# Optimization experiments

Measured on AMD Instinct MI355X. Metric: run time of the kernel, lower is better.

The kernel has to match this reference:

```python
import jax, jax.numpy as jnp
import numpy as np

NUM_CHANNELS = 512
B_DIM = 64
C_DIM = 16
N = 512
FEAT = NUM_CHANNELS * 4 * 4  # 8192


def setup_inputs() -> dict:
    key = jax.random.key(0)
    k1, k2 = jax.random.split(key)
    inp = jax.random.normal(k1, (N, NUM_CHANNELS, 4, 4), dtype=jnp.float32)
    T = jax.random.normal(k2, (FEAT, B_DIM * C_DIM), dtype=jnp.float32) * 0.1
    return {"inp": inp, "T": T}


def reference(inp, T):
    x = inp.reshape(-1, FEAT)                      # (N, 8192)
    M = (x @ T).reshape(-1, B_DIM, C_DIM)          # (N, B, C)
    # pairwise L1 distance over C: (N, N, B)
    dist = jnp.sum(jnp.abs(M[:, None, :, :] - M[None, :, :, :]), axis=-1)
    o = jnp.sum(jnp.exp(-dist), axis=1)            # (N, B)
    return jnp.concatenate((x, o), axis=1)         # (N, 8192 + B)
```

## Files before the change

kernel.cpp:

```cpp
#include <hip/hip_runtime.h>

#define NROWS 512
#define FEAT  8192
#define BDIM  64
#define CDIM  16
#define MCOLS 1024
#define OUTC  8256
#define KSPLIT 16
#define KCHUNK (FEAT / KSPLIT)
#define MSIZE  (NROWS * MCOLS)

typedef __bf16 bf16x8 __attribute__((ext_vector_type(8)));
typedef float  floatx4 __attribute__((ext_vector_type(4)));

#define AS1 __attribute__((address_space(1)))
#define AS3 __attribute__((address_space(3)))

static __device__ __forceinline__ void gload16(const void* g, void* l) {
    __builtin_amdgcn_global_load_lds((AS1 void*)(g), (AS3 void*)(l), 16, 0, 0);
}

static __device__ __forceinline__ unsigned short f2bf(float f) {
    unsigned int x = __builtin_bit_cast(unsigned int, f);
    unsigned int r = (x + 0x7FFFu + ((x >> 16) & 1u)) >> 16;
    return (unsigned short)r;
}

__global__ __launch_bounds__(256) void prep_kernel(const float* __restrict__ x,
                                                   const float* __restrict__ T,
                                                   unsigned short* __restrict__ xb,
                                                   unsigned short* __restrict__ Tt,
                                                   float* __restrict__ out) {
    __shared__ float lds[64][65];
    int bid = blockIdx.x, t = threadIdx.x;
    if (bid < 4096) {
        int gid = bid * 256 + t;
        float4 v = *(const float4*)(x + (size_t)gid * 4);
        ushort4 u;
        u.x = f2bf(v.x); u.y = f2bf(v.y); u.z = f2bf(v.z); u.w = f2bf(v.w);
        *(ushort4*)(xb + (size_t)gid * 4) = u;
        int row = gid >> 11, col4 = gid & 2047;
        *(float4*)(out + (size_t)row * OUTC + col4 * 4) = v;
    } else {
        int b2 = bid - 4096;
        int kt = b2 & 127, nt = b2 >> 7;
        int kk = t >> 2, q = t & 3;
#pragma unroll
        for (int p = 0; p < 4; ++p) {
            int c4 = q + p * 4;
            float4 v = *(const float4*)(T + (size_t)(kt * 64 + kk) * MCOLS + nt * 64 + c4 * 4);
            lds[kk][c4 * 4 + 0] = v.x; lds[kk][c4 * 4 + 1] = v.y;
            lds[kk][c4 * 4 + 2] = v.z; lds[kk][c4 * 4 + 3] = v.w;
        }
        __syncthreads();
        int nr = t >> 2, ck = t & 3;
        unsigned int w[8];
#pragma unroll
        for (int j = 0; j < 8; ++j) {
            unsigned int lo = f2bf(lds[ck * 16 + j * 2 + 0][nr]);
            unsigned int hi = f2bf(lds[ck * 16 + j * 2 + 1][nr]);
            w[j] = lo | (hi << 16);
        }
        uint4* dst = (uint4*)(Tt + (size_t)(nt * 64 + nr) * FEAT + kt * 64 + ck * 16);
        dst[0] = make_uint4(w[0], w[1], w[2], w[3]);
        dst[1] = make_uint4(w[4], w[5], w[6], w[7]);
    }
}

__global__ __launch_bounds__(256, 2) void gemm_kernel(const unsigned short* __restrict__ xb,
                                                      const unsigned short* __restrict__ Tt,
                                                      float* __restrict__ Mp) {
    __shared__ __align__(16) unsigned short ldsA[128 * 32];
    __shared__ __align__(16) unsigned short ldsB[128 * 32];

    int bid = blockIdx.x;
    int mt = bid & 3, nt = (bid >> 2) & 7, ks = bid >> 5;
    int m0 = mt * 128, n0 = nt * 128, kbase = ks * KCHUNK;
    int t = threadIdx.x, w = t >> 6, l = t & 63;

    int r0 = w * 32 + (l >> 2);
    int c  = (l & 3) ^ ((r0 >> 1) & 3);
    const unsigned short* gA0 = xb + (size_t)(m0 + r0) * FEAT + kbase + c * 8;
    const unsigned short* gB0 = Tt + (size_t)(n0 + r0) * FEAT + kbase + c * 8;
    unsigned short* lA0 = &ldsA[w * 1024];
    unsigned short* lA1 = &ldsA[w * 1024 + 512];
    unsigned short* lB0 = &ldsB[w * 1024];
    unsigned short* lB1 = &ldsB[w * 1024 + 512];

    int wr = w >> 1, wc = w & 1, fm = l & 15, fq = l >> 4;
    int swz = (fm >> 1) & 3;
    const unsigned short* pa[4];
    const unsigned short* pb[4];
#pragma unroll
    for (int a = 0; a < 4; ++a)
        pa[a] = &ldsA[(wr * 64 + a * 16 + fm) * 32 + ((fq ^ swz) * 8)];
#pragma unroll
    for (int b = 0; b < 4; ++b)
        pb[b] = &ldsB[(wc * 64 + b * 16 + fm) * 32 + ((fq ^ swz) * 8)];

    floatx4 acc[4][4] = {};

    for (int kk = 0; kk < KCHUNK; kk += 32) {
        if (kk) __syncthreads();
        gload16(gA0 + kk,             lA0);
        gload16(gA0 + 16 * FEAT + kk, lA1);
        gload16(gB0 + kk,             lB0);
        gload16(gB0 + 16 * FEAT + kk, lB1);
        __syncthreads();
        bf16x8 af[4], bfr[4];
#pragma unroll
        for (int a = 0; a < 4; ++a) af[a] = *(const bf16x8*)pa[a];
#pragma unroll
        for (int b = 0; b < 4; ++b) bfr[b] = *(const bf16x8*)pb[b];
#pragma unroll
        for (int a = 0; a < 4; ++a)
#pragma unroll
            for (int b = 0; b < 4; ++b)
                acc[a][b] = __builtin_amdgcn_mfma_f32_16x16x32_bf16(af[a], bfr[b], acc[a][b], 0, 0, 0);
    }

    float* outp = Mp + (size_t)ks * MSIZE;
    int gr0 = m0 + wr * 64, gc0 = n0 + wc * 64;
#pragma unroll
    for (int a = 0; a < 4; ++a)
#pragma unroll
        for (int r = 0; r < 4; ++r) {
            int row = gr0 + a * 16 + fq * 4 + r;
#pragma unroll
            for (int b = 0; b < 4; ++b)
                outp[(size_t)row * MCOLS + gc0 + b * 16 + fm] = acc[a][b][r];
        }
}

__global__ __launch_bounds__(256) void reduce_kernel(const float* __restrict__ Mp,
                                                     float* __restrict__ Ms) {
    int gid = blockIdx.x * 256 + threadIdx.x;
    const float4* p = (const float4*)Mp;
    float4 s = p[gid];
#pragma unroll
    for (int k = 1; k < KSPLIT; ++k) {
        float4 v = p[(size_t)k * (MSIZE / 4) + gid];
        s.x += v.x; s.y += v.y; s.z += v.z; s.w += v.w;
    }
    ((float4*)Ms)[gid] = s;
}

__global__ __launch_bounds__(256) void pairwise_kernel(const float* __restrict__ Ms,
                                                       float* __restrict__ out) {
    __shared__ float ldsM[NROWS * 20];
    __shared__ float partial[4][64];
    int b = blockIdx.x & 63, it = blockIdx.x >> 6;
    int t = threadIdx.x;
#pragma unroll
    for (int p = 0; p < 8; ++p) {
        int idx = t + p * 256;
        int j = idx >> 2, c4 = idx & 3;
        float4 v = *(const float4*)(Ms + (size_t)j * MCOLS + b * CDIM + c4 * 4);
        *(float4*)&ldsM[j * 20 + c4 * 4] = v;
    }
    __syncthreads();

    int lane = t & 63, w = t >> 6;
    int i = it * 64 + lane;
    float mi[CDIM];
#pragma unroll
    for (int cc = 0; cc < CDIM; ++cc) mi[cc] = ldsM[i * 20 + cc];

    float acc = 0.0f;
    for (int jj = w * 128; jj < w * 128 + 128; ++jj) {
        float d = 0.0f;
#pragma unroll
        for (int cc = 0; cc < CDIM; ++cc) d += fabsf(mi[cc] - ldsM[jj * 20 + cc]);
        acc += __expf(-d);
    }
    partial[w][lane] = acc;
    __syncthreads();
    if (w == 0) {
        float o = partial[0][lane] + partial[1][lane] + partial[2][lane] + partial[3][lane];
        out[(size_t)i * OUTC + FEAT + b] = o;
    }
}

extern "C" void kernel_launch(void* const* d_in, const int* in_sizes, int n_in,
                              void* d_out, int out_size, void* d_ws, size_t ws_size,
                              hipStream_t stream) {
    const float* x = (const float*)d_in[0];
    const float* T = (const float*)d_in[1];
    float* out = (float*)d_out;

    unsigned short* xb = (unsigned short*)d_ws;
    unsigned short* Tt = (unsigned short*)((char*)d_ws + (8u << 20));
    float*          Mp = (float*)((char*)d_ws + (24u << 20));
    float*          Ms = (float*)((char*)d_ws + (56u << 20));

    prep_kernel<<<6144, 256, 0, stream>>>(x, T, xb, Tt, out);
    gemm_kernel<<<512, 256, 0, stream>>>(xb, Tt, Mp);
    reduce_kernel<<<512, 256, 0, stream>>>(Mp, Ms);
    pairwise_kernel<<<512, 256, 0, stream>>>(Ms, out);
}
```

Baseline: 137.1 us.

## Fuse all stages into one cooperative kernel with grid syncs

Merges the prep, GEMM, split-K reduce and pairwise stages into a single persistent cooperative kernel of 256 blocks by 512 threads, separated by grid-wide barriers, to remove three kernel launch gaps. The GEMM split-K factor is halved to 8, which cuts partial-sum traffic and the reduce work but leaves each block a longer K loop. The fallback path keeps four separate launches. Grid.sync barriers add their own overhead, and using only 256 blocks may underfill the device during the prep and pairwise phases.

```diff
diff --git a/kernel.cpp b/kernel.cpp
--- a/kernel.cpp
+++ b/kernel.cpp
@@ -1,4 +1,7 @@
 #include <hip/hip_runtime.h>
+#include <hip/hip_cooperative_groups.h>
+
+namespace cg = cooperative_groups;
 
 #define NROWS 512
 #define FEAT  8192
@@ -6,9 +9,11 @@
 #define CDIM  16
 #define MCOLS 1024
 #define OUTC  8256
-#define KSPLIT 16
+#define KSPLIT 8
 #define KCHUNK (FEAT / KSPLIT)
 #define MSIZE  (NROWS * MCOLS)
+
+#define SMEM_BYTES 43008
 
 typedef __bf16 bf16x8 __attribute__((ext_vector_type(8)));
 typedef float  floatx4 __attribute__((ext_vector_type(4)));
@@ -26,115 +31,114 @@
     return (unsigned short)r;
 }
 
-__global__ __launch_bounds__(256) void prep_kernel(const float* __restrict__ x,
-                                                   const float* __restrict__ T,
-                                                   unsigned short* __restrict__ xb,
-                                                   unsigned short* __restrict__ Tt,
-                                                   float* __restrict__ out) {
-    __shared__ float lds[64][65];
-    int bid = blockIdx.x, t = threadIdx.x;
-    if (bid < 4096) {
-        int gid = bid * 256 + t;
+
+static __device__ __forceinline__ void prep_body(
+        int bid, int t, char* smem,
+        const float* __restrict__ x, const float* __restrict__ T,
+        unsigned short* __restrict__ xb, unsigned short* __restrict__ Tt,
+        float* __restrict__ out) {
+#pragma unroll
+    for (int u = 0; u < 8; ++u) {
+        int gid = bid * 4096 + u * 512 + t;
         float4 v = *(const float4*)(x + (size_t)gid * 4);
-        ushort4 u;
-        u.x = f2bf(v.x); u.y = f2bf(v.y); u.z = f2bf(v.z); u.w = f2bf(v.w);
-        *(ushort4*)(xb + (size_t)gid * 4) = u;
+        ushort4 uu;
+        uu.x = f2bf(v.x); uu.y = f2bf(v.y); uu.z = f2bf(v.z); uu.w = f2bf(v.w);
+        *(ushort4*)(xb + (size_t)gid * 4) = uu;
         int row = gid >> 11, col4 = gid & 2047;
         *(float4*)(out + (size_t)row * OUTC + col4 * 4) = v;
-    } else {
-        int b2 = bid - 4096;
-        int kt = b2 & 127, nt = b2 >> 7;
-        int kk = t >> 2, q = t & 3;
+    }
+    float (*lds)[64][65] = (float (*)[64][65])smem;
+    int sub = t >> 8, tt = t & 255;
+    for (int u = 0; u < 4; ++u) {
+        int tile = bid * 8 + u * 2 + sub;
+        int kt = tile & 127, nt = tile >> 7;
+        __syncthreads();
+        int kk = tt >> 2, q = tt & 3;
 #pragma unroll
         for (int p = 0; p < 4; ++p) {
             int c4 = q + p * 4;
             float4 v = *(const float4*)(T + (size_t)(kt * 64 + kk) * MCOLS + nt * 64 + c4 * 4);
-            lds[kk][c4 * 4 + 0] = v.x; lds[kk][c4 * 4 + 1] = v.y;
-            lds[kk][c4 * 4 + 2] = v.z; lds[kk][c4 * 4 + 3] = v.w;
+            lds[sub][kk][c4 * 4 + 0] = v.x; lds[sub][kk][c4 * 4 + 1] = v.y;
+            lds[sub][kk][c4 * 4 + 2] = v.z; lds[sub][kk][c4 * 4 + 3] = v.w;
         }
         __syncthreads();
-        int nr = t >> 2, ck = t & 3;
-        unsigned int w[8];
+        int nr = tt >> 2, ck = tt & 3;
+        unsigned int wv[8];
 #pragma unroll
         for (int j = 0; j < 8; ++j) {
-            unsigned int lo = f2bf(lds[ck * 16 + j * 2 + 0][nr]);
-            unsigned int hi = f2bf(lds[ck * 16 + j * 2 + 1][nr]);
-            w[j] = lo | (hi << 16);
+            unsigned int lo = f2bf(lds[sub][ck * 16 + j * 2 + 0][nr]);
+            unsigned int hi = f2bf(lds[sub][ck * 16 + j * 2 + 1][nr]);
+            wv[j] = lo | (hi << 16);
         }
         uint4* dst = (uint4*)(Tt + (size_t)(nt * 64 + nr) * FEAT + kt * 64 + ck * 16);
-        dst[0] = make_uint4(w[0], w[1], w[2], w[3]);
-        dst[1] = make_uint4(w[4], w[5], w[6], w[7]);
-    }
-}
-
-__global__ __launch_bounds__(256, 2) void gemm_kernel(const unsigned short* __restrict__ xb,
-                                                      const unsigned short* __restrict__ Tt,
-                                                      float* __restrict__ Mp) {
-    __shared__ __align__(16) unsigned short ldsA[128 * 32];
-    __shared__ __align__(16) unsigned short ldsB[128 * 32];
-
-    int bid = blockIdx.x;
+        dst[0] = make_uint4(wv[0], wv[1], wv[2], wv[3]);
+        dst[1] = make_uint4(wv[4], wv[5], wv[6], wv[7]);
+    }
+}
+
+static __device__ __forceinline__ void gemm_body(
+        int bid, int t, char* smem,
+        const unsigned short* __restrict__ xb, const unsigned short* __restrict__ Tt,
+        float* __restrict__ Mp) {
+    unsigned short* ldsA = (unsigned short*)smem;
+    unsigned short* ldsB = (unsigned short*)(smem + 8192);
     int mt = bid & 3, nt = (bid >> 2) & 7, ks = bid >> 5;
     int m0 = mt * 128, n0 = nt * 128, kbase = ks * KCHUNK;
-    int t = threadIdx.x, w = t >> 6, l = t & 63;
-
-    int r0 = w * 32 + (l >> 2);
+    int w = t >> 6, l = t & 63;
+
+    int r0 = w * 16 + (l >> 2);
     int c  = (l & 3) ^ ((r0 >> 1) & 3);
-    const unsigned short* gA0 = xb + (size_t)(m0 + r0) * FEAT + kbase + c * 8;
-    const unsigned short* gB0 = Tt + (size_t)(n0 + r0) * FEAT + kbase + c * 8;
-    unsigned short* lA0 = &ldsA[w * 1024];
-    unsigned short* lA1 = &ldsA[w * 1024 + 512];
-    unsigned short* lB0 = &ldsB[w * 1024];
-    unsigned short* lB1 = &ldsB[w * 1024 + 512];
-
-    int wr = w >> 1, wc = w & 1, fm = l & 15, fq = l >> 4;
+    const unsigned short* gA = xb + (size_t)(m0 + r0) * FEAT + kbase + c * 8;
+    const unsigned short* gB = Tt + (size_t)(n0 + r0) * FEAT + kbase + c * 8;
+    unsigned short* lA = ldsA + w * 512;
+    unsigned short* lB = ldsB + w * 512;
+
+    int wr = w >> 2, wc = w & 3, fm = l & 15, fq = l >> 4;
     int swz = (fm >> 1) & 3;
     const unsigned short* pa[4];
-    const unsigned short* pb[4];
+    const unsigned short* pb[2];
 #pragma unroll
     for (int a = 0; a < 4; ++a)
-        pa[a] = &ldsA[(wr * 64 + a * 16 + fm) * 32 + ((fq ^ swz) * 8)];
-#pragma unroll
-    for (int b = 0; b < 4; ++b)
-        pb[b] = &ldsB[(wc * 64 + b * 16 + fm) * 32 + ((fq ^ swz) * 8)];
-
-    floatx4 acc[4][4] = {};
+        pa[a] = ldsA + (wr * 64 + a * 16 + fm) * 32 + ((fq ^ swz) * 8);
+#pragma unroll
+    for (int b = 0; b < 2; ++b)
+        pb[b] = ldsB + (wc * 32 + b * 16 + fm) * 32 + ((fq ^ swz) * 8);
+
+    floatx4 acc[4][2] = {};
 
     for (int kk = 0; kk < KCHUNK; kk += 32) {
-        if (kk) __syncthreads();
-        gload16(gA0 + kk,             lA0);
-        gload16(gA0 + 16 * FEAT + kk, lA1);
-        gload16(gB0 + kk,             lB0);
-        gload16(gB0 + 16 * FEAT + kk, lB1);
-        __syncthreads();
-        bf16x8 af[4], bfr[4];
+        __syncthreads();
+        gload16(gA + kk, lA);
+        gload16(gB + kk, lB);
+        __syncthreads();
+        bf16x8 af[4], bfr[2];
 #pragma unroll
         for (int a = 0; a < 4; ++a) af[a] = *(const bf16x8*)pa[a];
 #pragma unroll
-        for (int b = 0; b < 4; ++b) bfr[b] = *(const bf16x8*)pb[b];
+        for (int b = 0; b < 2; ++b) bfr[b] = *(const bf16x8*)pb[b];
 #pragma unroll
         for (int a = 0; a < 4; ++a)
 #pragma unroll
-            for (int b = 0; b < 4; ++b)
+            for (int b = 0; b < 2; ++b)
                 acc[a][b] = __builtin_amdgcn_mfma_f32_16x16x32_bf16(af[a], bfr[b], acc[a][b], 0, 0, 0);
     }
 
     float* outp = Mp + (size_t)ks * MSIZE;
-    int gr0 = m0 + wr * 64, gc0 = n0 + wc * 64;
+    int gr0 = m0 + wr * 64, gc0 = n0 + wc * 32;
 #pragma unroll
     for (int a = 0; a < 4; ++a)
 #pragma unroll
         for (int r = 0; r < 4; ++r) {
             int row = gr0 + a * 16 + fq * 4 + r;
 #pragma unroll
-            for (int b = 0; b < 4; ++b)
+            for (int b = 0; b < 2; ++b)
                 outp[(size_t)row * MCOLS + gc0 + b * 16 + fm] = acc[a][b][r];
         }
 }
 
-__global__ __launch_bounds__(256) void reduce_kernel(const float* __restrict__ Mp,
-                                                     float* __restrict__ Ms) {
-    int gid = blockIdx.x * 256 + threadIdx.x;
+static __device__ __forceinline__ void reduce_body(
+        int bid, int t, const float* __restrict__ Mp, float* __restrict__ Ms) {
+    int gid = bid * 512 + t;
     const float4* p = (const float4*)Mp;
     float4 s = p[gid];
 #pragma unroll
@@ -145,29 +149,29 @@
     ((float4*)Ms)[gid] = s;
 }
 
-__global__ __launch_bounds__(256) void pairwise_kernel(const float* __restrict__ Ms,
-                                                       float* __restrict__ out) {
-    __shared__ float ldsM[NROWS * 20];
-    __shared__ float partial[4][64];
-    int b = blockIdx.x & 63, it = blockIdx.x >> 6;
-    int t = threadIdx.x;
-#pragma unroll
-    for (int p = 0; p < 8; ++p) {
-        int idx = t + p * 256;
+static __device__ __forceinline__ void pairwise_body(
+        int bid, int t, char* smem,
+        const float* __restrict__ Ms, float* __restrict__ out) {
+    float* ldsM = (float*)smem;
+    float (*partial)[64] = (float (*)[64])(smem + 40960);
+    int b = bid & 63, itp = bid >> 6;
+#pragma unroll
+    for (int p = 0; p < 4; ++p) {
+        int idx = t + p * 512;
         int j = idx >> 2, c4 = idx & 3;
         float4 v = *(const float4*)(Ms + (size_t)j * MCOLS + b * CDIM + c4 * 4);
         *(float4*)&ldsM[j * 20 + c4 * 4] = v;
     }
     __syncthreads();
 
-    int lane = t & 63, w = t >> 6;
-    int i = it * 64 + lane;
+    int lane = t & 63, w = t >> 6, g = t >> 8, wg = (t >> 6) & 3;
+    int i = (itp * 2 + g) * 64 + lane;
     float mi[CDIM];
 #pragma unroll
     for (int cc = 0; cc < CDIM; ++cc) mi[cc] = ldsM[i * 20 + cc];
 
     float acc = 0.0f;
-    for (int jj = w * 128; jj < w * 128 + 128; ++jj) {
+    for (int jj = wg * 128; jj < wg * 128 + 128; ++jj) {
         float d = 0.0f;
 #pragma unroll
         for (int cc = 0; cc < CDIM; ++cc) d += fabsf(mi[cc] - ldsM[jj * 20 + cc]);
@@ -175,10 +179,57 @@
     }
     partial[w][lane] = acc;
     __syncthreads();
-    if (w == 0) {
-        float o = partial[0][lane] + partial[1][lane] + partial[2][lane] + partial[3][lane];
-        out[(size_t)i * OUTC + FEAT + b] = o;
-    }
+    if ((t & 255) < 64) {
+        int ii = (itp * 2 + g) * 64 + (t & 63);
+        float o = partial[g * 4 + 0][t & 63] + partial[g * 4 + 1][t & 63] +
+                  partial[g * 4 + 2][t & 63] + partial[g * 4 + 3][t & 63];
+        out[(size_t)ii * OUTC + FEAT + b] = o;
+    }
+}
+
+__global__ __launch_bounds__(512, 2) void fused_kernel(
+        const float* __restrict__ x, const float* __restrict__ T,
+        unsigned short* __restrict__ xb, unsigned short* __restrict__ Tt,
+        float* __restrict__ Mp, float* __restrict__ Ms,
+        float* __restrict__ out) {
+    __shared__ __align__(16) char smem[SMEM_BYTES];
+    cg::grid_group grid = cg::this_grid();
+    int bid = blockIdx.x, t = threadIdx.x;
+
+    prep_body(bid, t, smem, x, T, xb, Tt, out);
+    __threadfence();
+    grid.sync();
+    gemm_body(bid, t, smem, xb, Tt, Mp);
+    __threadfence();
+    grid.sync();
+    reduce_body(bid, t, Mp, Ms);
+    __threadfence();
+    grid.sync();
+    pairwise_body(bid, t, smem, Ms, out);
+}
+
+__global__ __launch_bounds__(512, 2) void k_prep(const float* __restrict__ x,
+                                                 const float* __restrict__ T,
+                                                 unsigned short* __restrict__ xb,
+                                                 unsigned short* __restrict__ Tt,
+                                                 float* __restrict__ out) {
+    __shared__ __align__(16) char smem[33280];
+    prep_body(blockIdx.x, threadIdx.x, smem, x, T, xb, Tt, out);
+}
+__global__ __launch_bounds__(512, 2) void k_gemm(const unsigned short* __restrict__ xb,
+                                                 const unsigned short* __restrict__ Tt,
+                                                 float* __restrict__ Mp) {
+    __shared__ __align__(16) char smem[16384];
+    gemm_body(blockIdx.x, threadIdx.x, smem, xb, Tt, Mp);
+}
+__global__ __launch_bounds__(512, 2) void k_reduce(const float* __restrict__ Mp,
+                                                   float* __restrict__ Ms) {
+    reduce_body(blockIdx.x, threadIdx.x, Mp, Ms);
+}
+__global__ __launch_bounds__(512, 2) void k_pair(const float* __restrict__ Ms,
+                                                 float* __restrict__ out) {
+    __shared__ __align__(16) char smem[43008];
+    pairwise_body(blockIdx.x, threadIdx.x, smem, Ms, out);
 }
 
 extern "C" void kernel_launch(void* const* d_in, const int* in_sizes, int n_in,
@@ -191,10 +242,23 @@
     unsigned short* xb = (unsigned short*)d_ws;
     unsigned short* Tt = (unsigned short*)((char*)d_ws + (8u << 20));
     float*          Mp = (float*)((char*)d_ws + (24u << 20));
-    float*          Ms = (float*)((char*)d_ws + (56u << 20));
-
-    prep_kernel<<<6144, 256, 0, stream>>>(x, T, xb, Tt, out);
-    gemm_kernel<<<512, 256, 0, stream>>>(xb, Tt, Mp);
-    reduce_kernel<<<512, 256, 0, stream>>>(Mp, Ms);
-    pairwise_kernel<<<512, 256, 0, stream>>>(Ms, out);
-}
+    float*          Ms = (float*)((char*)d_ws + (40u << 20));
+
+    int dev = 0; hipGetDevice(&dev);
+    int coop = 0; hipDeviceGetAttribute(&coop, hipDeviceAttributeCooperativeLaunch, dev);
+    int ncu = 0;  hipDeviceGetAttribute(&ncu, hipDeviceAttributeMultiprocessorCount, dev);
+    int nb = 0;
+    hipOccupancyMaxActiveBlocksPerMultiprocessor(&nb, (const void*)fused_kernel, 512, 0);
+
+    if (coop && nb > 0 && nb * ncu >= 256) {
+        void* args[] = {(void*)&x, (void*)&T, (void*)&xb, (void*)&Tt,
+                        (void*)&Mp, (void*)&Ms, (void*)&out};
+        hipLaunchCooperativeKernel((const void*)fused_kernel, dim3(256), dim3(512),
+                                   args, 0, stream);
+    } else {
+        k_prep<<<256, 512, 0, stream>>>(x, T, xb, Tt, out);
+        k_gemm<<<256, 512, 0, stream>>>(xb, Tt, Mp);
+        k_reduce<<<256, 512, 0, stream>>>(Mp, Ms);
+        k_pair<<<256, 512, 0, stream>>>(Ms, out);
+    }
+}
```

After: 408.8 us. 2.98x slower.
